# Kernel optimization log

Hardware: AMD Instinct MI355X
Metric: run time of the kernel (lower is better)

## Reference

```python
import jax, jax.numpy as jnp
import numpy as np

B, T, C, H = 2, 2048, 1024, 16
D = C // H  # head dim = 64


def setup_inputs() -> dict:
    key = jax.random.key(0)
    ks = jax.random.split(key, 5)
    s_in = 1.0 / np.sqrt(C)
    return {
        "x": jax.random.normal(ks[0], (B, T, C), dtype=jnp.float32),
        "W_qkv": jax.random.uniform(ks[1], (C, 3 * C), jnp.float32, -s_in, s_in),
        "b_qkv": jax.random.uniform(ks[2], (3 * C,), jnp.float32, -s_in, s_in),
        "W_proj": jax.random.uniform(ks[3], (C, C), jnp.float32, -s_in, s_in),
        "b_proj": jax.random.uniform(ks[4], (C,), jnp.float32, -s_in, s_in),
    }


def reference(x, W_qkv, b_qkv, W_proj, b_proj):
    Bx, Tx, Cx = x.shape
    qkv = x @ W_qkv + b_qkv                      # [B,T,3C]
    q, k, v = jnp.split(qkv, 3, axis=2)          # each [B,T,C]
    # [B,T,C] -> [B,H,T,D]
    q = q.reshape(Bx, Tx, H, D).transpose(0, 2, 1, 3)
    k = k.reshape(Bx, Tx, H, D).transpose(0, 2, 1, 3)
    v = v.reshape(Bx, Tx, H, D).transpose(0, 2, 1, 3)
    scale = 1.0 / jnp.sqrt(jnp.asarray(D, dtype=x.dtype))
    scores = jnp.einsum("bhqd,bhkd->bhqk", q, k) * scale  # [B,H,T,T]
    causal = jnp.tril(jnp.ones((Tx, Tx), dtype=bool))
    scores = jnp.where(causal, scores, jnp.finfo(x.dtype).min)
    attn = jax.nn.softmax(scores, axis=-1)
    y = jnp.einsum("bhqk,bhkd->bhqd", attn, v)   # [B,H,T,D]
    y = y.transpose(0, 2, 1, 3).reshape(Bx, Tx, Cx)
    return y @ W_proj + b_proj
```

## Files before the change

### kernel.cpp

```cpp
#include <hip/hip_runtime.h>
#include <hip/hip_bf16.h>

#define Bb 2
#define Tt 2048
#define Cc 1024
#define Hh 16
#define Dd 64

typedef __bf16 bf16x8 __attribute__((ext_vector_type(8)));
typedef __bf16 bf16x4 __attribute__((ext_vector_type(4)));
typedef float f32x4 __attribute__((ext_vector_type(4)));

#define MFMA16(a, b, c) __builtin_amdgcn_mfma_f32_16x16x32_bf16((a), (b), (c), 0, 0, 0)

__device__ __forceinline__ bf16x8 ldg8(const __hip_bfloat16* p) {
  return *reinterpret_cast<const bf16x8*>(p);
}
__device__ __forceinline__ bf16x8 lds8(const __bf16* p) {
  return *reinterpret_cast<const bf16x8*>(p);
}

__device__ __forceinline__ void load_lds16(const __hip_bfloat16* g, __hip_bfloat16* l) {
  __builtin_amdgcn_global_load_lds(
      (const __attribute__((address_space(1))) void*)g,
      (__attribute__((address_space(3))) void*)l, 16, 0, 0);
}

__global__ __launch_bounds__(256) void cvt_f32_bf16(
    const float* __restrict__ in, __hip_bfloat16* __restrict__ out, int n) {
  const int i = (blockIdx.x * 256 + threadIdx.x) * 4;
  if (i + 3 < n) {
    const float4 v = *reinterpret_cast<const float4*>(in + i);
    out[i + 0] = __float2bfloat16(v.x);
    out[i + 1] = __float2bfloat16(v.y);
    out[i + 2] = __float2bfloat16(v.z);
    out[i + 3] = __float2bfloat16(v.w);
  }
}

__global__ __launch_bounds__(256) void transpose_cvt(
    const float* __restrict__ in, __hip_bfloat16* __restrict__ out,
    int R, int Cn) {
  __shared__ float tile[32][33];
  const int c0 = blockIdx.x * 32, r0 = blockIdx.y * 32;
  const int tx = threadIdx.x, ty = threadIdx.y;
#pragma unroll
  for (int i = 0; i < 32; i += 8)
    tile[ty + i][tx] = in[(size_t)(r0 + ty + i) * Cn + c0 + tx];
  __syncthreads();
#pragma unroll
  for (int i = 0; i < 32; i += 8)
    out[(size_t)(c0 + ty + i) * R + r0 + tx] = __float2bfloat16(tile[tx][ty + i]);
}

__global__ __launch_bounds__(256) void qkv_gemm(
    const __hip_bfloat16* __restrict__ x, const __hip_bfloat16* __restrict__ WT,
    const float* __restrict__ bias,
    __hip_bfloat16* __restrict__ Q, __hip_bfloat16* __restrict__ Kd,
    __hip_bfloat16* __restrict__ VT) {
  __shared__ __hip_bfloat16 As[128 * 32];
  __shared__ __hip_bfloat16 Bs[128 * 32];
  const int tid = threadIdx.x;
  const int wave = tid >> 6, lane = tid & 63;
  const int l16 = lane & 15, quad = lane >> 4;
  const int m0 = blockIdx.y * 128, n0 = blockIdx.x * 128;
  const int wm = (wave >> 1) * 64, wn = (wave & 1) * 64;

  const int srow = wave * 32 + (lane >> 2);
  const int kseg = (lane & 3) * 8;

  f32x4 acc[4][4] = {};

  for (int k0 = 0; k0 < Cc; k0 += 32) {
    __syncthreads();
#pragma unroll
    for (int j = 0; j < 2; ++j) {
      load_lds16(x + (size_t)(m0 + srow + j * 16) * Cc + k0 + kseg,
                 As + (wave * 32 + j * 16) * 32);
      load_lds16(WT + (size_t)(n0 + srow + j * 16) * Cc + k0 + kseg,
                 Bs + (wave * 32 + j * 16) * 32);
    }
    __syncthreads();

    bf16x8 af[4], bfr[4];
#pragma unroll
    for (int i = 0; i < 4; ++i) {
      af[i] = ldg8(As + (wm + i * 16 + l16) * 32 + quad * 8);
      bfr[i] = ldg8(Bs + (wn + i * 16 + l16) * 32 + quad * 8);
    }
#pragma unroll
    for (int i = 0; i < 4; ++i)
#pragma unroll
      for (int jn = 0; jn < 4; ++jn)
        acc[i][jn] = MFMA16(af[i], bfr[jn], acc[i][jn]);
  }

  const int sect = n0 >> 10;
#pragma unroll
  for (int jn = 0; jn < 4; ++jn) {
    const int n = n0 + wn + jn * 16 + l16;
    const float bv = bias[n];
    const int ch = n & 1023;
    const int h = ch >> 6, d = ch & 63;
#pragma unroll
    for (int i = 0; i < 4; ++i) {
#pragma unroll
      for (int r = 0; r < 4; ++r) {
        const int m = m0 + wm + i * 16 + quad * 4 + r;
        const int b = m >> 11, t = m & 2047;
        const __hip_bfloat16 o = __float2bfloat16(acc[i][jn][r] + bv);
        const int bh = b * Hh + h;
        if (sect == 0)      Q[((size_t)bh * Tt + t) * Dd + d] = o;
        else if (sect == 1) Kd[((size_t)bh * Tt + t) * Dd + d] = o;
        else                VT[((size_t)bh * Dd + d) * Tt + t] = o;
      }
    }
  }
}

__global__ __launch_bounds__(256) void attn(
    const __hip_bfloat16* __restrict__ Q, const __hip_bfloat16* __restrict__ K,
    const __hip_bfloat16* __restrict__ VT, __hip_bfloat16* __restrict__ O) {
  const int tid = threadIdx.x;
  const int wave = tid >> 6, lane = tid & 63;
  const int l16 = lane & 15, quad = lane >> 4;
  const int bh = blockIdx.z * Hh + blockIdx.y;

  const __hip_bfloat16* Qh = Q + (size_t)bh * Tt * Dd;
  const __hip_bfloat16* Kh = K + (size_t)bh * Tt * Dd;
  const __hip_bfloat16* Vh = VT + (size_t)bh * Dd * Tt;
  __hip_bfloat16* Oh = O + (size_t)bh * Tt * Dd;

  __shared__ __align__(16) __bf16 Kt[64 * 72];
  __shared__ __align__(16) __bf16 Vt[64 * 72];
  __shared__ __align__(16) __bf16 Pt[4][16 * 72];

  const float SC = 0.18033688011112042f;
  const int skey = tid >> 3, sd = (tid & 7) * 8;

  const int qbA = blockIdx.x;
  const int qbB = (Tt / 64 - 1) - qbA;
  const int qrowA = qbA * 64 + wave * 16 + l16;
  const int qrowB = qbB * 64 + wave * 16 + l16;

  const bf16x8 qA0 = ldg8(Qh + (size_t)qrowA * Dd + quad * 8);
  const bf16x8 qA1 = ldg8(Qh + (size_t)qrowA * Dd + 32 + quad * 8);
  const bf16x8 qB0 = ldg8(Qh + (size_t)qrowB * Dd + quad * 8);
  const bf16x8 qB1 = ldg8(Qh + (size_t)qrowB * Dd + 32 + quad * 8);

  f32x4 oA[4] = {}, oB[4] = {};
  float mA = -INFINITY, lA = 0.f, mB = -INFINITY, lB = 0.f;

  const int nkB = qbB + 1;

  bf16x8 ka = ldg8(Kh + (size_t)skey * Dd + sd);
  bf16x8 kb = ldg8(Kh + (size_t)(32 + skey) * Dd + sd);
  bf16x8 va = ldg8(Vh + (size_t)skey * Tt + sd);
  bf16x8 vb = ldg8(Vh + (size_t)(32 + skey) * Tt + sd);

  auto process = [&](const bf16x8& q0f, const bf16x8& q1f, f32x4* oacc,
                     float& m_s, float& l_s, int qrow, int k0, bool diag) {
    f32x4 st[4];
#pragma unroll
    for (int kt = 0; kt < 4; ++kt) {
      const __bf16* kr = &Kt[(kt * 16 + l16) * 72 + quad * 8];
      f32x4 z = {};
      z = MFMA16(lds8(kr), q0f, z);
      st[kt] = MFMA16(lds8(kr + 32), q1f, z);
    }
    float v[16];
    float mx = -INFINITY;
    if (diag) {
#pragma unroll
      for (int kt = 0; kt < 4; ++kt)
#pragma unroll
        for (int r = 0; r < 4; ++r) {
          const int key = k0 + kt * 16 + quad * 4 + r;
          const float val = (key <= qrow) ? st[kt][r] * SC : -INFINITY;
          v[kt * 4 + r] = val;
          mx = fmaxf(mx, val);
        }
    } else {
#pragma unroll
      for (int kt = 0; kt < 4; ++kt)
#pragma unroll
        for (int r = 0; r < 4; ++r) {
          const float val = st[kt][r] * SC;
          v[kt * 4 + r] = val;
          mx = fmaxf(mx, val);
        }
    }
    mx = fmaxf(mx, __shfl_xor(mx, 16, 64));
    mx = fmaxf(mx, __shfl_xor(mx, 32, 64));
    const float mnew = fmaxf(m_s, mx);
    const float alpha = exp2f(m_s - mnew);
    m_s = mnew;
    float rs = 0.f;
#pragma unroll
    for (int kt = 0; kt < 4; ++kt) {
      bf16x4 pk;
#pragma unroll
      for (int r = 0; r < 4; ++r) {
        const float p = exp2f(v[kt * 4 + r] - mnew);
        rs += p;
        pk[r] = (__bf16)p;
      }
      *reinterpret_cast<bf16x4*>(&Pt[wave][l16 * 72 + kt * 16 + quad * 4]) = pk;
    }
    rs += __shfl_xor(rs, 16, 64);
    rs += __shfl_xor(rs, 32, 64);
    l_s = l_s * alpha + rs;
#pragma unroll
    for (int dt = 0; dt < 4; ++dt) oacc[dt] *= alpha;
    const bf16x8 pf0 = lds8(&Pt[wave][l16 * 72 + quad * 8]);
    const bf16x8 pf1 = lds8(&Pt[wave][l16 * 72 + 32 + quad * 8]);
#pragma unroll
    for (int dt = 0; dt < 4; ++dt) {
      const __bf16* vr = &Vt[(dt * 16 + l16) * 72];
      oacc[dt] = MFMA16(lds8(vr + quad * 8), pf0, oacc[dt]);
      oacc[dt] = MFMA16(lds8(vr + 32 + quad * 8), pf1, oacc[dt]);
    }
  };

  for (int kt0 = 0; kt0 < nkB; ++kt0) {
    const int k0 = kt0 * 64;
    __syncthreads();
    *reinterpret_cast<bf16x8*>(&Kt[skey * 72 + sd]) = ka;
    *reinterpret_cast<bf16x8*>(&Kt[(32 + skey) * 72 + sd]) = kb;
    *reinterpret_cast<bf16x8*>(&Vt[skey * 72 + sd]) = va;
    *reinterpret_cast<bf16x8*>(&Vt[(32 + skey) * 72 + sd]) = vb;
    if (kt0 + 1 < nkB) {
      const int k1 = k0 + 64;
      ka = ldg8(Kh + (size_t)(k1 + skey) * Dd + sd);
      kb = ldg8(Kh + (size_t)(k1 + 32 + skey) * Dd + sd);
      va = ldg8(Vh + (size_t)skey * Tt + k1 + sd);
      vb = ldg8(Vh + (size_t)(32 + skey) * Tt + k1 + sd);
    }
    __syncthreads();

    process(qB0, qB1, oB, mB, lB, qrowB, k0, kt0 == qbB);
    if (kt0 <= qbA) process(qA0, qA1, oA, mA, lA, qrowA, k0, kt0 == qbA);
  }

  const float invA = 1.f / lA, invB = 1.f / lB;
#pragma unroll
  for (int dt = 0; dt < 4; ++dt) {
    bf16x4 ovA, ovB;
#pragma unroll
    for (int r = 0; r < 4; ++r) {
      ovA[r] = (__bf16)(oA[dt][r] * invA);
      ovB[r] = (__bf16)(oB[dt][r] * invB);
    }
    *reinterpret_cast<bf16x4*>(&Oh[(size_t)qrowA * Dd + dt * 16 + quad * 4]) = ovA;
    *reinterpret_cast<bf16x4*>(&Oh[(size_t)qrowB * Dd + dt * 16 + quad * 4]) = ovB;
  }
}

__global__ __launch_bounds__(256) void proj_gemm(
    const __hip_bfloat16* __restrict__ O, const __hip_bfloat16* __restrict__ WT,
    const float* __restrict__ bias, float* __restrict__ out) {
  __shared__ __hip_bfloat16 As[128 * 32];
  __shared__ __hip_bfloat16 Bs[128 * 32];
  const int tid = threadIdx.x;
  const int wave = tid >> 6, lane = tid & 63;
  const int l16 = lane & 15, quad = lane >> 4;
  const int m0 = blockIdx.y * 128, n0 = blockIdx.x * 128;
  const int wm = (wave >> 1) * 64, wn = (wave & 1) * 64;

  const int srow = wave * 32 + (lane >> 2);
  const int kseg = (lane & 3) * 8;

  f32x4 acc[4][4] = {};

  for (int k0 = 0; k0 < Cc; k0 += 32) {
    const int k = k0 + kseg;
    const int h = k >> 6, d = k & 63;
    __syncthreads();
#pragma unroll
    for (int j = 0; j < 2; ++j) {
      const int m = m0 + srow + j * 16;
      const int b = m >> 11, t = m & 2047;
      load_lds16(O + ((size_t)(b * Hh + h) * Tt + t) * Dd + d,
                 As + (wave * 32 + j * 16) * 32);
      load_lds16(WT + (size_t)(n0 + srow + j * 16) * Cc + k0 + kseg,
                 Bs + (wave * 32 + j * 16) * 32);
    }
    __syncthreads();

    bf16x8 af[4], bfr[4];
#pragma unroll
    for (int i = 0; i < 4; ++i) {
      af[i] = ldg8(As + (wm + i * 16 + l16) * 32 + quad * 8);
      bfr[i] = ldg8(Bs + (wn + i * 16 + l16) * 32 + quad * 8);
    }
#pragma unroll
    for (int i = 0; i < 4; ++i)
#pragma unroll
      for (int jn = 0; jn < 4; ++jn)
        acc[i][jn] = MFMA16(af[i], bfr[jn], acc[i][jn]);
  }

#pragma unroll
  for (int jn = 0; jn < 4; ++jn) {
    const int n = n0 + wn + jn * 16 + l16;
    const float bv = bias[n];
#pragma unroll
    for (int i = 0; i < 4; ++i)
#pragma unroll
      for (int r = 0; r < 4; ++r) {
        const int m = m0 + wm + i * 16 + quad * 4 + r;
        out[(size_t)m * Cc + n] = acc[i][jn][r] + bv;
      }
  }
}

extern "C" void kernel_launch(void* const* d_in, const int* in_sizes, int n_in,
                              void* d_out, int out_size, void* d_ws, size_t ws_size,
                              hipStream_t stream) {
  const float* x      = (const float*)d_in[0];
  const float* W_qkv  = (const float*)d_in[1];
  const float* b_qkv  = (const float*)d_in[2];
  const float* W_proj = (const float*)d_in[3];
  const float* b_proj = (const float*)d_in[4];
  float* out = (float*)d_out;

  __hip_bfloat16* ws = (__hip_bfloat16*)d_ws;
  const size_t NBHTD = (size_t)Bb * Hh * Tt * Dd;
  __hip_bfloat16* Qw  = ws;
  __hip_bfloat16* Kw  = ws + NBHTD;
  __hip_bfloat16* VTw = ws + 2 * NBHTD;
  __hip_bfloat16* Ow  = ws + 3 * NBHTD;
  __hip_bfloat16* xb  = ws + 4 * NBHTD;
  __hip_bfloat16* WTqkv  = xb + NBHTD;
  __hip_bfloat16* WTproj = WTqkv + (size_t)3 * Cc * Cc;

  cvt_f32_bf16<<<dim3(4096), dim3(256), 0, stream>>>(x, xb, Bb * Tt * Cc);
  transpose_cvt<<<dim3(96, 32), dim3(32, 8), 0, stream>>>(W_qkv, WTqkv, Cc, 3 * Cc);
  transpose_cvt<<<dim3(32, 32), dim3(32, 8), 0, stream>>>(W_proj, WTproj, Cc, Cc);
  qkv_gemm<<<dim3(24, 32), 256, 0, stream>>>(xb, WTqkv, b_qkv, Qw, Kw, VTw);
  attn<<<dim3(Tt / 128, Hh, Bb), 256, 0, stream>>>(Qw, Kw, VTw, Ow);
  proj_gemm<<<dim3(8, 32), 256, 0, stream>>>(Ow, WTproj, b_proj, out);
}
```

Measured before the change: 202.0 us.

## Split attention into 32-row query tiles with 2-wave blocks and fold scale into exp

Measured after the change: 236.6 us. +17.1%, slower.

```diff
diff --git a/kernel.cpp b/kernel.cpp
--- a/kernel.cpp
+++ b/kernel.cpp
@@ -118,7 +118,7 @@
   }
 }
 
-__global__ __launch_bounds__(256) void attn(
+__global__ __launch_bounds__(128, 3) void attn(
     const __hip_bfloat16* __restrict__ Q, const __hip_bfloat16* __restrict__ K,
     const __hip_bfloat16* __restrict__ VT, __hip_bfloat16* __restrict__ O) {
   const int tid = threadIdx.x;
@@ -133,15 +133,14 @@
 
   __shared__ __align__(16) __bf16 Kt[64 * 72];
   __shared__ __align__(16) __bf16 Vt[64 * 72];
-  __shared__ __align__(16) __bf16 Pt[4][16 * 72];
+  __shared__ __align__(16) __bf16 Pt[2][16 * 72];
 
   const float SC = 0.18033688011112042f;
-  const int skey = tid >> 3, sd = (tid & 7) * 8;
 
   const int qbA = blockIdx.x;
-  const int qbB = (Tt / 64 - 1) - qbA;
-  const int qrowA = qbA * 64 + wave * 16 + l16;
-  const int qrowB = qbB * 64 + wave * 16 + l16;
+  const int qbB = 63 - qbA;
+  const int qrowA = qbA * 32 + wave * 16 + l16;
+  const int qrowB = qbB * 32 + wave * 16 + l16;
 
   const bf16x8 qA0 = ldg8(Qh + (size_t)qrowA * Dd + quad * 8);
   const bf16x8 qA1 = ldg8(Qh + (size_t)qrowA * Dd + 32 + quad * 8);
@@ -151,12 +150,19 @@
   f32x4 oA[4] = {}, oB[4] = {};
   float mA = -INFINITY, lA = 0.f, mB = -INFINITY, lB = 0.f;
 
-  const int nkB = qbB + 1;
-
-  bf16x8 ka = ldg8(Kh + (size_t)skey * Dd + sd);
-  bf16x8 kb = ldg8(Kh + (size_t)(32 + skey) * Dd + sd);
-  bf16x8 va = ldg8(Vh + (size_t)skey * Tt + sd);
-  bf16x8 vb = ldg8(Vh + (size_t)(32 + skey) * Tt + sd);
+  const int nkA = qbA / 2 + 1;
+  const int nkB = qbB / 2 + 1;
+
+  const int srow0 = tid >> 3;
+  const int sseg = (tid & 7) * 8;
+
+  bf16x8 kpre[4], vpre[4];
+#pragma unroll
+  for (int s = 0; s < 4; ++s) {
+    const int row = s * 16 + srow0;
+    kpre[s] = ldg8(Kh + (size_t)row * Dd + sseg);
+    vpre[s] = ldg8(Vh + (size_t)row * Tt + sseg);
+  }
 
   auto process = [&](const bf16x8& q0f, const bf16x8& q1f, f32x4* oacc,
                      float& m_s, float& l_s, int qrow, int k0, bool diag) {
@@ -176,7 +182,7 @@
 #pragma unroll
         for (int r = 0; r < 4; ++r) {
           const int key = k0 + kt * 16 + quad * 4 + r;
-          const float val = (key <= qrow) ? st[kt][r] * SC : -INFINITY;
+          const float val = (key <= qrow) ? st[kt][r] : -INFINITY;
           v[kt * 4 + r] = val;
           mx = fmaxf(mx, val);
         }
@@ -185,7 +191,7 @@
       for (int kt = 0; kt < 4; ++kt)
 #pragma unroll
         for (int r = 0; r < 4; ++r) {
-          const float val = st[kt][r] * SC;
+          const float val = st[kt][r];
           v[kt * 4 + r] = val;
           mx = fmaxf(mx, val);
         }
@@ -193,7 +199,8 @@
     mx = fmaxf(mx, __shfl_xor(mx, 16, 64));
     mx = fmaxf(mx, __shfl_xor(mx, 32, 64));
     const float mnew = fmaxf(m_s, mx);
-    const float alpha = exp2f(m_s - mnew);
+    const float alpha = exp2f((m_s - mnew) * SC);
+    const float msc = mnew * SC;
     m_s = mnew;
     float rs = 0.f;
 #pragma unroll
@@ -201,7 +208,7 @@
       bf16x4 pk;
 #pragma unroll
       for (int r = 0; r < 4; ++r) {
-        const float p = exp2f(v[kt * 4 + r] - mnew);
+        const float p = exp2f(__builtin_fmaf(v[kt * 4 + r], SC, -msc));
         rs += p;
         pk[r] = (__bf16)p;
       }
@@ -225,21 +232,25 @@
   for (int kt0 = 0; kt0 < nkB; ++kt0) {
     const int k0 = kt0 * 64;
     __syncthreads();
-    *reinterpret_cast<bf16x8*>(&Kt[skey * 72 + sd]) = ka;
-    *reinterpret_cast<bf16x8*>(&Kt[(32 + skey) * 72 + sd]) = kb;
-    *reinterpret_cast<bf16x8*>(&Vt[skey * 72 + sd]) = va;
-    *reinterpret_cast<bf16x8*>(&Vt[(32 + skey) * 72 + sd]) = vb;
+#pragma unroll
+    for (int s = 0; s < 4; ++s) {
+      const int row = s * 16 + srow0;
+      *reinterpret_cast<bf16x8*>(&Kt[row * 72 + sseg]) = kpre[s];
+      *reinterpret_cast<bf16x8*>(&Vt[row * 72 + sseg]) = vpre[s];
+    }
     if (kt0 + 1 < nkB) {
       const int k1 = k0 + 64;
-      ka = ldg8(Kh + (size_t)(k1 + skey) * Dd + sd);
-      kb = ldg8(Kh + (size_t)(k1 + 32 + skey) * Dd + sd);
-      va = ldg8(Vh + (size_t)skey * Tt + k1 + sd);
-      vb = ldg8(Vh + (size_t)(32 + skey) * Tt + k1 + sd);
-    }
-    __syncthreads();
-
-    process(qB0, qB1, oB, mB, lB, qrowB, k0, kt0 == qbB);
-    if (kt0 <= qbA) process(qA0, qA1, oA, mA, lA, qrowA, k0, kt0 == qbA);
+#pragma unroll
+      for (int s = 0; s < 4; ++s) {
+        const int row = s * 16 + srow0;
+        kpre[s] = ldg8(Kh + (size_t)(k1 + row) * Dd + sseg);
+        vpre[s] = ldg8(Vh + (size_t)row * Tt + k1 + sseg);
+      }
+    }
+    __syncthreads();
+
+    process(qB0, qB1, oB, mB, lB, qrowB, k0, kt0 == nkB - 1);
+    if (kt0 < nkA) process(qA0, qA1, oA, mA, lA, qrowA, k0, kt0 == nkA - 1);
   }
 
   const float invA = 1.f / lA, invB = 1.f / lB;
@@ -338,6 +349,6 @@
   transpose_cvt<<<dim3(96, 32), dim3(32, 8), 0, stream>>>(W_qkv, WTqkv, Cc, 3 * Cc);
   transpose_cvt<<<dim3(32, 32), dim3(32, 8), 0, stream>>>(W_proj, WTproj, Cc, Cc);
   qkv_gemm<<<dim3(24, 32), 256, 0, stream>>>(xb, WTqkv, b_qkv, Qw, Kw, VTw);
-  attn<<<dim3(Tt / 128, Hh, Bb), 256, 0, stream>>>(Qw, Kw, VTw, Ow);
+  attn<<<dim3(32, Hh, Bb), 128, 0, stream>>>(Qw, Kw, VTw, Ow);
   proj_gemm<<<dim3(8, 32), 256, 0, stream>>>(Ow, WTproj, b_proj, out);
 }
```

## Interleave both query blocks per key tile to share K/V fragment loads

Applied to the files above, without the earlier changes.

New measurement: 204.2 us. No clear change (+1.1%).

```diff
diff --git a/kernel.cpp b/kernel.cpp
--- a/kernel.cpp
+++ b/kernel.cpp
@@ -118,7 +118,7 @@
   }
 }
 
-__global__ __launch_bounds__(256) void attn(
+__global__ __launch_bounds__(256, 2) void attn(
     const __hip_bfloat16* __restrict__ Q, const __hip_bfloat16* __restrict__ K,
     const __hip_bfloat16* __restrict__ VT, __hip_bfloat16* __restrict__ O) {
   const int tid = threadIdx.x;
@@ -133,7 +133,7 @@
 
   __shared__ __align__(16) __bf16 Kt[64 * 72];
   __shared__ __align__(16) __bf16 Vt[64 * 72];
-  __shared__ __align__(16) __bf16 Pt[4][16 * 72];
+  __shared__ __align__(16) __bf16 Pt[4][2][16 * 72];
 
   const float SC = 0.18033688011112042f;
   const int skey = tid >> 3, sd = (tid & 7) * 8;
@@ -157,70 +157,6 @@
   bf16x8 kb = ldg8(Kh + (size_t)(32 + skey) * Dd + sd);
   bf16x8 va = ldg8(Vh + (size_t)skey * Tt + sd);
   bf16x8 vb = ldg8(Vh + (size_t)(32 + skey) * Tt + sd);
-
-  auto process = [&](const bf16x8& q0f, const bf16x8& q1f, f32x4* oacc,
-                     float& m_s, float& l_s, int qrow, int k0, bool diag) {
-    f32x4 st[4];
-#pragma unroll
-    for (int kt = 0; kt < 4; ++kt) {
-      const __bf16* kr = &Kt[(kt * 16 + l16) * 72 + quad * 8];
-      f32x4 z = {};
-      z = MFMA16(lds8(kr), q0f, z);
-      st[kt] = MFMA16(lds8(kr + 32), q1f, z);
-    }
-    float v[16];
-    float mx = -INFINITY;
-    if (diag) {
-#pragma unroll
-      for (int kt = 0; kt < 4; ++kt)
-#pragma unroll
-        for (int r = 0; r < 4; ++r) {
-          const int key = k0 + kt * 16 + quad * 4 + r;
-          const float val = (key <= qrow) ? st[kt][r] * SC : -INFINITY;
-          v[kt * 4 + r] = val;
-          mx = fmaxf(mx, val);
-        }
-    } else {
-#pragma unroll
-      for (int kt = 0; kt < 4; ++kt)
-#pragma unroll
-        for (int r = 0; r < 4; ++r) {
-          const float val = st[kt][r] * SC;
-          v[kt * 4 + r] = val;
-          mx = fmaxf(mx, val);
-        }
-    }
-    mx = fmaxf(mx, __shfl_xor(mx, 16, 64));
-    mx = fmaxf(mx, __shfl_xor(mx, 32, 64));
-    const float mnew = fmaxf(m_s, mx);
-    const float alpha = exp2f(m_s - mnew);
-    m_s = mnew;
-    float rs = 0.f;
-#pragma unroll
-    for (int kt = 0; kt < 4; ++kt) {
-      bf16x4 pk;
-#pragma unroll
-      for (int r = 0; r < 4; ++r) {
-        const float p = exp2f(v[kt * 4 + r] - mnew);
-        rs += p;
-        pk[r] = (__bf16)p;
-      }
-      *reinterpret_cast<bf16x4*>(&Pt[wave][l16 * 72 + kt * 16 + quad * 4]) = pk;
-    }
-    rs += __shfl_xor(rs, 16, 64);
-    rs += __shfl_xor(rs, 32, 64);
-    l_s = l_s * alpha + rs;
-#pragma unroll
-    for (int dt = 0; dt < 4; ++dt) oacc[dt] *= alpha;
-    const bf16x8 pf0 = lds8(&Pt[wave][l16 * 72 + quad * 8]);
-    const bf16x8 pf1 = lds8(&Pt[wave][l16 * 72 + 32 + quad * 8]);
-#pragma unroll
-    for (int dt = 0; dt < 4; ++dt) {
-      const __bf16* vr = &Vt[(dt * 16 + l16) * 72];
-      oacc[dt] = MFMA16(lds8(vr + quad * 8), pf0, oacc[dt]);
-      oacc[dt] = MFMA16(lds8(vr + 32 + quad * 8), pf1, oacc[dt]);
-    }
-  };
 
   for (int kt0 = 0; kt0 < nkB; ++kt0) {
     const int k0 = kt0 * 64;
@@ -238,8 +174,134 @@
     }
     __syncthreads();
 
-    process(qB0, qB1, oB, mB, lB, qrowB, k0, kt0 == qbB);
-    if (kt0 <= qbA) process(qA0, qA1, oA, mA, lA, qrowA, k0, kt0 == qbA);
+    const bool doA = (kt0 <= qbA);
+    const bool diagB = (kt0 == qbB), diagA = (kt0 == qbA);
+
+    f32x4 stB[4], stA[4];
+#pragma unroll
+    for (int kt = 0; kt < 4; ++kt) {
+      const __bf16* kr = &Kt[(kt * 16 + l16) * 72 + quad * 8];
+      const bf16x8 k0f = lds8(kr), k1f = lds8(kr + 32);
+      f32x4 zb = {};
+      zb = MFMA16(k0f, qB0, zb);
+      stB[kt] = MFMA16(k1f, qB1, zb);
+      if (doA) {
+        f32x4 za = {};
+        za = MFMA16(k0f, qA0, za);
+        stA[kt] = MFMA16(k1f, qA1, za);
+      }
+    }
+
+    float vB[16], mxB = -INFINITY;
+    if (diagB) {
+#pragma unroll
+      for (int kt = 0; kt < 4; ++kt)
+#pragma unroll
+        for (int r = 0; r < 4; ++r) {
+          const int key = k0 + kt * 16 + quad * 4 + r;
+          const float val = (key <= qrowB) ? stB[kt][r] : -INFINITY;
+          vB[kt * 4 + r] = val;
+          mxB = fmaxf(mxB, val);
+        }
+    } else {
+#pragma unroll
+      for (int kt = 0; kt < 4; ++kt)
+#pragma unroll
+        for (int r = 0; r < 4; ++r) {
+          const float val = stB[kt][r];
+          vB[kt * 4 + r] = val;
+          mxB = fmaxf(mxB, val);
+        }
+    }
+    mxB = fmaxf(mxB, __shfl_xor(mxB, 16, 64));
+    mxB = fmaxf(mxB, __shfl_xor(mxB, 32, 64));
+    const float mnewB = fmaxf(mB, mxB);
+    const float alphaB = exp2f((mB - mnewB) * SC);
+    const float mscB = mnewB * SC;
+    mB = mnewB;
+    float rsB = 0.f;
+#pragma unroll
+    for (int kt = 0; kt < 4; ++kt) {
+      bf16x4 pk;
+#pragma unroll
+      for (int r = 0; r < 4; ++r) {
+        const float p = exp2f(__builtin_fmaf(vB[kt * 4 + r], SC, -mscB));
+        rsB += p;
+        pk[r] = (__bf16)p;
+      }
+      *reinterpret_cast<bf16x4*>(&Pt[wave][0][l16 * 72 + kt * 16 + quad * 4]) = pk;
+    }
+    rsB += __shfl_xor(rsB, 16, 64);
+    rsB += __shfl_xor(rsB, 32, 64);
+    lB = lB * alphaB + rsB;
+
+    float alphaA = 1.f;
+    if (doA) {
+      float vA[16], mxA = -INFINITY;
+      if (diagA) {
+#pragma unroll
+        for (int kt = 0; kt < 4; ++kt)
+#pragma unroll
+          for (int r = 0; r < 4; ++r) {
+            const int key = k0 + kt * 16 + quad * 4 + r;
+            const float val = (key <= qrowA) ? stA[kt][r] : -INFINITY;
+            vA[kt * 4 + r] = val;
+            mxA = fmaxf(mxA, val);
+          }
+      } else {
+#pragma unroll
+        for (int kt = 0; kt < 4; ++kt)
+#pragma unroll
+          for (int r = 0; r < 4; ++r) {
+            const float val = stA[kt][r];
+            vA[kt * 4 + r] = val;
+            mxA = fmaxf(mxA, val);
+          }
+      }
+      mxA = fmaxf(mxA, __shfl_xor(mxA, 16, 64));
+      mxA = fmaxf(mxA, __shfl_xor(mxA, 32, 64));
+      const float mnewA = fmaxf(mA, mxA);
+      alphaA = exp2f((mA - mnewA) * SC);
+      const float mscA = mnewA * SC;
+      mA = mnewA;
+      float rsA = 0.f;
+#pragma unroll
+      for (int kt = 0; kt < 4; ++kt) {
+        bf16x4 pk;
+#pragma unroll
+        for (int r = 0; r < 4; ++r) {
+          const float p = exp2f(__builtin_fmaf(vA[kt * 4 + r], SC, -mscA));
+          rsA += p;
+          pk[r] = (__bf16)p;
+        }
+        *reinterpret_cast<bf16x4*>(&Pt[wave][1][l16 * 72 + kt * 16 + quad * 4]) = pk;
+      }
+      rsA += __shfl_xor(rsA, 16, 64);
+      rsA += __shfl_xor(rsA, 32, 64);
+      lA = lA * alphaA + rsA;
+    }
+
+#pragma unroll
+    for (int dt = 0; dt < 4; ++dt) oB[dt] *= alphaB;
+    if (doA) {
+#pragma unroll
+      for (int dt = 0; dt < 4; ++dt) oA[dt] *= alphaA;
+    }
+    const bf16x8 pB0 = lds8(&Pt[wave][0][l16 * 72 + quad * 8]);
+    const bf16x8 pB1 = lds8(&Pt[wave][0][l16 * 72 + 32 + quad * 8]);
+    const bf16x8 pA0 = lds8(&Pt[wave][1][l16 * 72 + quad * 8]);
+    const bf16x8 pA1 = lds8(&Pt[wave][1][l16 * 72 + 32 + quad * 8]);
+#pragma unroll
+    for (int dt = 0; dt < 4; ++dt) {
+      const __bf16* vr = &Vt[(dt * 16 + l16) * 72];
+      const bf16x8 v0f = lds8(vr + quad * 8), v1f = lds8(vr + 32 + quad * 8);
+      oB[dt] = MFMA16(v0f, pB0, oB[dt]);
+      oB[dt] = MFMA16(v1f, pB1, oB[dt]);
+      if (doA) {
+        oA[dt] = MFMA16(v0f, pA0, oA[dt]);
+        oA[dt] = MFMA16(v1f, pA1, oA[dt]);
+      }
+    }
   }
 
   const float invA = 1.f / lA, invB = 1.f / lB;
```
